# Kernel tuning notes

Measured on AMD Instinct MI355X. Metric: run time of the kernel, lower is better.

Reference implementation:

```python
import jax, jax.numpy as jnp
import numpy as np

HEADS = 8
DIM_HEAD = 32
SCALE = DIM_HEAD ** -0.5


def setup_inputs() -> dict:
    key = jax.random.key(0)
    k1, k2, k3 = jax.random.split(key, 3)
    B, H, W, C = 16, 64, 64, 256
    hidden = HEADS * DIM_HEAD  # 256
    x = jax.random.normal(k1, (B, H, W, C), dtype=jnp.float32)
    # 1x1 convs with no bias == dense matmuls over channel dim (glorot-ish scale)
    w_qkv = jax.random.normal(k2, (C, 3 * hidden), dtype=jnp.float32) * (1.0 / np.sqrt(C))
    w_out = jax.random.normal(k3, (hidden, C), dtype=jnp.float32) * (1.0 / np.sqrt(hidden))
    return {"x": x, "w_qkv": w_qkv, "w_out": w_out}


def reference(x, w_qkv, w_out):
    B, H, W, C = x.shape
    n = H * W
    # to_qkv: 1x1 conv, no bias
    qkv = jnp.einsum('bhwc,cf->bhwf', x, w_qkv)  # [B,H,W,3*hidden]
    q, k, v = jnp.split(qkv, 3, axis=-1)

    def to_heads(t):
        # 'b x y (h c) -> b h c (x y)'
        t = t.reshape(B, n, HEADS, DIM_HEAD)
        return jnp.transpose(t, (0, 2, 3, 1))  # [B, heads, dim_head, n]

    q, k, v = to_heads(q), to_heads(k), to_heads(v)
    q = jax.nn.softmax(q, axis=-2) * SCALE      # softmax over feature dim d
    k = jax.nn.softmax(k, axis=-1)              # softmax over spatial dim n
    context = jnp.einsum('bhdn,bhen->bhde', k, v)   # [B, heads, d, e]
    out = jnp.einsum('bhde,bhdn->bhen', context, q)  # [B, heads, e, n]
    # 'b h c (x y) -> b x y (h c)'
    out = jnp.transpose(out, (0, 3, 1, 2)).reshape(B, H, W, HEADS * DIM_HEAD)
    # to_out: 1x1 conv, no bias
    return jnp.einsum('bhwf,fc->bhwc', out, w_out)
```

## Files before the change

### kernel.cpp

```cpp
#include <hip/hip_runtime.h>

using short8 = __attribute__((ext_vector_type(8))) short;
using f32x4  = __attribute__((ext_vector_type(4))) float;

#define SCALE_Q 0.17677669529663687f
#define NCHUNK 16

__device__ __forceinline__ unsigned short f2bf(float f) {
  unsigned u = __float_as_uint(f);
  return (unsigned short)((u + 0x7FFFu + ((u >> 16) & 1u)) >> 16);
}
__device__ __forceinline__ float bf2f(unsigned h) { return __uint_as_float(h << 16); }

__device__ __forceinline__ void bf8_to_f(uint4 r, float* o) {
  o[0] = bf2f(r.x & 0xffffu); o[1] = bf2f(r.x >> 16);
  o[2] = bf2f(r.y & 0xffffu); o[3] = bf2f(r.y >> 16);
  o[4] = bf2f(r.z & 0xffffu); o[5] = bf2f(r.z >> 16);
  o[6] = bf2f(r.w & 0xffffu); o[7] = bf2f(r.w >> 16);
}

__global__ __launch_bounds__(256) void prep_kernel(
    const float* __restrict__ x, const float* __restrict__ wqkv, const float* __restrict__ wout,
    unsigned short* __restrict__ xb, unsigned short* __restrict__ wqkvT,
    unsigned short* __restrict__ woutT) {
  const int blk = blockIdx.x;
  if (blk < 16384) {
    const size_t i = ((size_t)blk * 256 + threadIdx.x) * 4;
    const float4 v = *(const float4*)(x + i);
    *(ushort4*)(xb + i) = make_ushort4(f2bf(v.x), f2bf(v.y), f2bf(v.z), f2bf(v.w));
  } else if (blk < 16384 + 768) {
    const int n = blk - 16384, k = threadIdx.x;
    wqkvT[n * 256 + k] = f2bf(wqkv[(size_t)k * 768 + n]);
  } else {
    const int c = blk - 16384 - 768, f = threadIdx.x;
    woutT[c * 256 + f] = f2bf(wout[(size_t)f * 256 + c]);
  }
}

__global__ __launch_bounds__(256) void gemm_qkv(
    const unsigned short* __restrict__ A, const unsigned short* __restrict__ BT,
    unsigned short* __restrict__ KV, unsigned short* __restrict__ QS) {
  constexpr int K = 256;
  __shared__ unsigned short As[128][40];
  __shared__ unsigned short Bs[128][40];
  const int cpx = (int)gridDim.x >> 3;
  const int lin = ((int)blockIdx.x & 7) * cpx + ((int)blockIdx.x >> 3);
  const int bn = lin % 6, bm = lin / 6;
  const int tid = threadIdx.x, lane = tid & 63, wid = tid >> 6;
  const int wr = wid >> 1, wc = wid & 1;
  const int fr = lane & 15, hi = lane >> 4, fk = hi * 8;
  f32x4 acc[4][4] = {};
  const size_t abase = (size_t)bm * 128 * K;
  const size_t bbase = (size_t)bn * 128 * K;

#pragma unroll
  for (int kt = 0; kt < K; kt += 32) {
#pragma unroll
    for (int c = tid; c < 512; c += 256) {
      const int row = c >> 2, kc = (c & 3) * 8;
      *(uint4*)&As[row][kc] = *(const uint4*)(A + abase + (size_t)row * K + kt + kc);
      *(uint4*)&Bs[row][kc] = *(const uint4*)(BT + bbase + (size_t)row * K + kt + kc);
    }
    __syncthreads();
    short8 af[4], bfv[4];
#pragma unroll
    for (int i = 0; i < 4; ++i) {
      af[i]  = *(const short8*)&As[wr * 64 + i * 16 + fr][fk];
      bfv[i] = *(const short8*)&Bs[wc * 64 + i * 16 + fr][fk];
    }
#pragma unroll
    for (int mi = 0; mi < 4; ++mi)
#pragma unroll
      for (int nj = 0; nj < 4; ++nj)
        acc[mi][nj] = __builtin_amdgcn_mfma_f32_16x16x32_bf16(bfv[nj], af[mi], acc[mi][nj], 0, 0, 0);
    __syncthreads();
  }

  const size_t r0 = (size_t)bm * 128 + wr * 64;
  if (bn < 2) {
    const int c0 = bn * 128 + wc * 64;
#pragma unroll
    for (int mi = 0; mi < 4; ++mi) {
      const size_t row = r0 + mi * 16 + fr;
#pragma unroll
      for (int p = 0; p < 2; ++p) {
        const f32x4 a0 = acc[mi][2 * p], a1 = acc[mi][2 * p + 1];
        float mx = fmaxf(fmaxf(fmaxf(a0[0], a0[1]), fmaxf(a0[2], a0[3])),
                         fmaxf(fmaxf(a1[0], a1[1]), fmaxf(a1[2], a1[3])));
        mx = fmaxf(mx, __shfl_xor(mx, 16, 64));
        mx = fmaxf(mx, __shfl_xor(mx, 32, 64));
        float e0[4], e1[4], s = 0.f;
#pragma unroll
        for (int r = 0; r < 4; ++r) {
          e0[r] = __expf(a0[r] - mx); e1[r] = __expf(a1[r] - mx);
          s += e0[r] + e1[r];
        }
        s += __shfl_xor(s, 16, 64);
        s += __shfl_xor(s, 32, 64);
        const float inv = SCALE_Q / s;
        unsigned short* qp = QS + row * 256 + c0 + p * 32 + hi * 4;
        *(ushort4*)(qp)      = make_ushort4(f2bf(e0[0]*inv), f2bf(e0[1]*inv), f2bf(e0[2]*inv), f2bf(e0[3]*inv));
        *(ushort4*)(qp + 16) = make_ushort4(f2bf(e1[0]*inv), f2bf(e1[1]*inv), f2bf(e1[2]*inv), f2bf(e1[3]*inv));
      }
    }
    return;
  }
  const int colbase = (bn - 2) * 128 + wc * 64;
#pragma unroll
  for (int mi = 0; mi < 4; ++mi) {
    const size_t row = r0 + mi * 16 + fr;
#pragma unroll
    for (int nj = 0; nj < 4; ++nj) {
      const int col0 = colbase + nj * 16 + hi * 4;
      const f32x4 v = acc[mi][nj];
      *(ushort4*)(KV + row * 512 + col0) =
          make_ushort4(f2bf(v[0]), f2bf(v[1]), f2bf(v[2]), f2bf(v[3]));
    }
  }
}

__global__ __launch_bounds__(256) void gemm_out(
    const unsigned short* __restrict__ A, const unsigned short* __restrict__ BT,
    float* __restrict__ D) {
  constexpr int K = 256;
  __shared__ unsigned short As[128][40];
  __shared__ unsigned short Bs[128][40];
  const int bn = blockIdx.x, bm = blockIdx.y, bz = blockIdx.z;
  const int tid = threadIdx.x, lane = tid & 63, wid = tid >> 6;
  const int wr = wid >> 1, wc = wid & 1;
  const int fr = lane & 15, hi = lane >> 4, fk = hi * 8;
  f32x4 acc[4][4] = {};
  const size_t abase = (size_t)bz * 4096 * 256 + (size_t)bm * 128 * K;
  const size_t bbase = (size_t)bz * 256 * 256 + (size_t)bn * 128 * K;

#pragma unroll
  for (int kt = 0; kt < K; kt += 32) {
#pragma unroll
    for (int c = tid; c < 512; c += 256) {
      const int row = c >> 2, kc = (c & 3) * 8;
      *(uint4*)&As[row][kc] = *(const uint4*)(A + abase + (size_t)row * K + kt + kc);
      *(uint4*)&Bs[row][kc] = *(const uint4*)(BT + bbase + (size_t)row * K + kt + kc);
    }
    __syncthreads();
    short8 af[4], bfv[4];
#pragma unroll
    for (int i = 0; i < 4; ++i) {
      af[i]  = *(const short8*)&As[wr * 64 + i * 16 + fr][fk];
      bfv[i] = *(const short8*)&Bs[wc * 64 + i * 16 + fr][fk];
    }
#pragma unroll
    for (int mi = 0; mi < 4; ++mi)
#pragma unroll
      for (int nj = 0; nj < 4; ++nj)
        acc[mi][nj] = __builtin_amdgcn_mfma_f32_16x16x32_bf16(bfv[nj], af[mi], acc[mi][nj], 0, 0, 0);
    __syncthreads();
  }

  const size_t r0 = (size_t)bm * 128 + wr * 64;
  const int colbase = bn * 128 + wc * 64;
  float* Dz = D + (size_t)bz * 4096 * 256;
#pragma unroll
  for (int mi = 0; mi < 4; ++mi) {
    const size_t row = r0 + mi * 16 + fr;
#pragma unroll
    for (int nj = 0; nj < 4; ++nj) {
      const f32x4 v = acc[mi][nj];
      *(float4*)(Dz + row * 256 + colbase + nj * 16 + hi * 4) =
          make_float4(v[0], v[1], v[2], v[3]);
    }
  }
}

__global__ __launch_bounds__(256) void ctx_part_kernel(const unsigned short* __restrict__ kv,
                                                       float* __restrict__ part,
                                                       float* __restrict__ spart) {
  const int blk = blockIdx.x;
  const int bh = blk >> 4, chunk = blk & 15;
  const int b = bh >> 3, h = bh & 7;
  const int tid = threadIdx.x, d = tid & 31, g = tid >> 5;
  const unsigned short* kbase =
      kv + (size_t)b * 4096 * 512 + h * 32 + (size_t)chunk * 256 * 512;
  const unsigned short* vbase = kbase + 256;

  __shared__ float ek[64][36], vv[64][36];
  float a0 = 0.f, a1 = 0.f, a2 = 0.f, a3 = 0.f, ssum = 0.f;
  const int e0 = g * 4;
  const int sn = tid >> 2, sc = (tid & 3) * 8;
  const unsigned short* kp0 = kbase + (size_t)sn * 512 + sc;
  const unsigned short* vp0 = vbase + (size_t)sn * 512 + sc;
  uint4 kr = *(const uint4*)kp0;
  uint4 vr = *(const uint4*)vp0;
  for (int n0 = 0; n0 < 256; n0 += 64) {
    float kf[8], vf[8];
    bf8_to_f(kr, kf); bf8_to_f(vr, vf);
    uint4 krn = kr, vrn = vr;
    if (n0 + 64 < 256) {
      krn = *(const uint4*)(kp0 + (size_t)(n0 + 64) * 512);
      vrn = *(const uint4*)(vp0 + (size_t)(n0 + 64) * 512);
    }
#pragma unroll
    for (int j = 0; j < 8; ++j) { ek[sn][sc + j] = __expf(kf[j]); vv[sn][sc + j] = vf[j]; }
    __syncthreads();
#pragma unroll 8
    for (int i = 0; i < 64; ++i) {
      const float kd = ek[i][d];
      const float4 v4 = *(const float4*)&vv[i][e0];
      ssum += kd;
      a0 += kd * v4.x; a1 += kd * v4.y; a2 += kd * v4.z; a3 += kd * v4.w;
    }
    __syncthreads();
    kr = krn; vr = vrn;
  }
  float* pp = part + ((size_t)chunk * 128 + bh) * 1024 + d * 32 + e0;
  pp[0] = a0; pp[1] = a1; pp[2] = a2; pp[3] = a3;
  if (g == 0) spart[((size_t)chunk * 128 + bh) * 32 + d] = ssum;
}

__global__ __launch_bounds__(256) void ctx_combine_kernel(const float* __restrict__ part,
                                                          const float* __restrict__ spart,
                                                          float* __restrict__ ctx) {
  const int bh = blockIdx.x, tid = threadIdx.x;
  __shared__ float sinv[32];
  if (tid < 32) {
    float s = 0.f;
#pragma unroll
    for (int c = 0; c < NCHUNK; ++c) s += spart[((size_t)c * 128 + bh) * 32 + tid];
    sinv[tid] = 1.0f / s;
  }
  __syncthreads();
  float4 acc = make_float4(0.f, 0.f, 0.f, 0.f);
#pragma unroll
  for (int c = 0; c < NCHUNK; ++c) {
    const float4 p = *(const float4*)(part + ((size_t)c * 128 + bh) * 1024 + tid * 4);
    acc.x += p.x; acc.y += p.y; acc.z += p.z; acc.w += p.w;
  }
  const float si = sinv[tid >> 3];
  float4* cp = (float4*)(ctx + (size_t)bh * 1024 + tid * 4);
  *cp = make_float4(acc.x * si, acc.y * si, acc.z * si, acc.w * si);
}

__global__ __launch_bounds__(256) void w2_kernel(const float* __restrict__ ctx,
                                                 const unsigned short* __restrict__ woutT,
                                                 unsigned short* __restrict__ W2T) {
  const int b = blockIdx.x >> 4, cg = blockIdx.x & 15;
  const int tid = threadIdx.x;
  __shared__ float cs[8 * 32 * 32];
  {
    const float4* src = (const float4*)(ctx + (size_t)b * 8192);
    float4* dst = (float4*)cs;
#pragma unroll
    for (int i = 0; i < 8; ++i) dst[tid + i * 256] = src[tid + i * 256];
  }
  __syncthreads();
  const int c = cg * 16 + (tid >> 4), chunk = tid & 15;
  const int h = chunk >> 1, d0 = (chunk & 1) * 16;
  float wf[32];
  {
    const uint4* wp = (const uint4*)(woutT + (size_t)c * 256 + h * 32);
    bf8_to_f(wp[0], wf + 0); bf8_to_f(wp[1], wf + 8);
    bf8_to_f(wp[2], wf + 16); bf8_to_f(wp[3], wf + 24);
  }
  unsigned short o[16];
#pragma unroll
  for (int dd = 0; dd < 16; ++dd) {
    const float* cp = cs + h * 1024 + (d0 + dd) * 32;
    float acc = 0.f;
#pragma unroll
    for (int e = 0; e < 32; ++e) acc += cp[e] * wf[e];
    o[dd] = f2bf(acc);
  }
  uint4* op = (uint4*)(W2T + ((size_t)b * 256 + c) * 256 + chunk * 16);
  op[0] = make_uint4((unsigned)o[0] | ((unsigned)o[1] << 16), (unsigned)o[2] | ((unsigned)o[3] << 16),
                     (unsigned)o[4] | ((unsigned)o[5] << 16), (unsigned)o[6] | ((unsigned)o[7] << 16));
  op[1] = make_uint4((unsigned)o[8] | ((unsigned)o[9] << 16), (unsigned)o[10] | ((unsigned)o[11] << 16),
                     (unsigned)o[12] | ((unsigned)o[13] << 16), (unsigned)o[14] | ((unsigned)o[15] << 16));
}

extern "C" void kernel_launch(void* const* d_in, const int* in_sizes, int n_in,
                              void* d_out, int out_size, void* d_ws, size_t ws_size,
                              hipStream_t stream) {
  const float* x     = (const float*)d_in[0];
  const float* wqkv  = (const float*)d_in[1];
  const float* wout  = (const float*)d_in[2];
  float* out = (float*)d_out;

  char* ws = (char*)d_ws;
  unsigned short* xb    = (unsigned short*)(ws);
  unsigned short* wqkvT = (unsigned short*)(ws + 33554432);
  unsigned short* woutT = (unsigned short*)(ws + 33947648);
  unsigned short* kv    = (unsigned short*)(ws + 34078720);
  float*          ctx   = (float*)        (ws + 101187584);
  unsigned short* qs    = (unsigned short*)(ws + 101711872);
  float*          part  = (float*)(ws);
  float*          spart = (float*)(ws + 8388608);
  unsigned short* W2T   = (unsigned short*)(ws + 12582912);

  prep_kernel<<<16384 + 768 + 256, 256, 0, stream>>>(x, wqkv, wout, xb, wqkvT, woutT);
  gemm_qkv<<<3072, 256, 0, stream>>>(xb, wqkvT, kv, qs);
  ctx_part_kernel<<<2048, 256, 0, stream>>>(kv, part, spart);
  ctx_combine_kernel<<<128, 256, 0, stream>>>(part, spart, ctx);
  w2_kernel<<<256, 256, 0, stream>>>(ctx, woutT, W2T);
  gemm_out<<<dim3(2, 32, 16), 256, 0, stream>>>(qs, W2T, out);
}
```

Measured before the change: 178.0 us.

## Double-buffer LDS tiles in both GEMMs with register prefetch of next K-tile

Both bf16 MFMA GEMMs now keep two LDS buffers and load the next K-slice from global memory into registers while the MFMAs run on the current slice. The registers are written to the other buffer afterwards, leaving one barrier per iteration instead of two. K becomes a runtime argument, so the K loop is no longer fully unrolled at compile time, and LDS use per block doubles, which may lower occupancy.

```diff
diff --git a/kernel.cpp b/kernel.cpp
--- a/kernel.cpp
+++ b/kernel.cpp
@@ -39,10 +39,9 @@
 
 __global__ __launch_bounds__(256) void gemm_qkv(
     const unsigned short* __restrict__ A, const unsigned short* __restrict__ BT,
-    unsigned short* __restrict__ KV, unsigned short* __restrict__ QS) {
-  constexpr int K = 256;
-  __shared__ unsigned short As[128][40];
-  __shared__ unsigned short Bs[128][40];
+    unsigned short* __restrict__ KV, unsigned short* __restrict__ QS, int K) {
+  __shared__ unsigned short As[2][128][40];
+  __shared__ unsigned short Bs[2][128][40];
   const int cpx = (int)gridDim.x >> 3;
   const int lin = ((int)blockIdx.x & 7) * cpx + ((int)blockIdx.x >> 3);
   const int bn = lin % 6, bm = lin / 6;
@@ -53,27 +52,42 @@
   const size_t abase = (size_t)bm * 128 * K;
   const size_t bbase = (size_t)bn * 128 * K;
 
-#pragma unroll
-  for (int kt = 0; kt < K; kt += 32) {
-#pragma unroll
-    for (int c = tid; c < 512; c += 256) {
-      const int row = c >> 2, kc = (c & 3) * 8;
-      *(uint4*)&As[row][kc] = *(const uint4*)(A + abase + (size_t)row * K + kt + kc);
-      *(uint4*)&Bs[row][kc] = *(const uint4*)(BT + bbase + (size_t)row * K + kt + kc);
-    }
-    __syncthreads();
+  const int srow = tid >> 2, skc = (tid & 3) * 8;
+  uint4 ra0, ra1, rb0, rb1;
+  const unsigned short* Ap = A + abase + (size_t)srow * K + skc;
+  const unsigned short* Bp = BT + bbase + (size_t)srow * K + skc;
+
+  ra0 = *(const uint4*)(Ap);            ra1 = *(const uint4*)(Ap + (size_t)64 * K);
+  rb0 = *(const uint4*)(Bp);            rb1 = *(const uint4*)(Bp + (size_t)64 * K);
+  *(uint4*)&As[0][srow][skc] = ra0;     *(uint4*)&As[0][srow + 64][skc] = ra1;
+  *(uint4*)&Bs[0][srow][skc] = rb0;     *(uint4*)&Bs[0][srow + 64][skc] = rb1;
+  __syncthreads();
+
+  const int ktiles = K >> 5;
+  int cur = 0;
+  for (int t = 0; t < ktiles; ++t) {
+    if (t + 1 < ktiles) {
+      const int kt = (t + 1) * 32;
+      ra0 = *(const uint4*)(Ap + kt);     ra1 = *(const uint4*)(Ap + (size_t)64 * K + kt);
+      rb0 = *(const uint4*)(Bp + kt);     rb1 = *(const uint4*)(Bp + (size_t)64 * K + kt);
+    }
     short8 af[4], bfv[4];
 #pragma unroll
     for (int i = 0; i < 4; ++i) {
-      af[i]  = *(const short8*)&As[wr * 64 + i * 16 + fr][fk];
-      bfv[i] = *(const short8*)&Bs[wc * 64 + i * 16 + fr][fk];
+      af[i]  = *(const short8*)&As[cur][wr * 64 + i * 16 + fr][fk];
+      bfv[i] = *(const short8*)&Bs[cur][wc * 64 + i * 16 + fr][fk];
     }
 #pragma unroll
     for (int mi = 0; mi < 4; ++mi)
 #pragma unroll
       for (int nj = 0; nj < 4; ++nj)
         acc[mi][nj] = __builtin_amdgcn_mfma_f32_16x16x32_bf16(bfv[nj], af[mi], acc[mi][nj], 0, 0, 0);
+    if (t + 1 < ktiles) {
+      *(uint4*)&As[cur ^ 1][srow][skc] = ra0;  *(uint4*)&As[cur ^ 1][srow + 64][skc] = ra1;
+      *(uint4*)&Bs[cur ^ 1][srow][skc] = rb0;  *(uint4*)&Bs[cur ^ 1][srow + 64][skc] = rb1;
+    }
     __syncthreads();
+    cur ^= 1;
   }
 
   const size_t r0 = (size_t)bm * 128 + wr * 64;
@@ -121,10 +135,9 @@
 
 __global__ __launch_bounds__(256) void gemm_out(
     const unsigned short* __restrict__ A, const unsigned short* __restrict__ BT,
-    float* __restrict__ D) {
-  constexpr int K = 256;
-  __shared__ unsigned short As[128][40];
-  __shared__ unsigned short Bs[128][40];
+    float* __restrict__ D, int K) {
+  __shared__ unsigned short As[2][128][40];
+  __shared__ unsigned short Bs[2][128][40];
   const int bn = blockIdx.x, bm = blockIdx.y, bz = blockIdx.z;
   const int tid = threadIdx.x, lane = tid & 63, wid = tid >> 6;
   const int wr = wid >> 1, wc = wid & 1;
@@ -133,27 +146,42 @@
   const size_t abase = (size_t)bz * 4096 * 256 + (size_t)bm * 128 * K;
   const size_t bbase = (size_t)bz * 256 * 256 + (size_t)bn * 128 * K;
 
-#pragma unroll
-  for (int kt = 0; kt < K; kt += 32) {
-#pragma unroll
-    for (int c = tid; c < 512; c += 256) {
-      const int row = c >> 2, kc = (c & 3) * 8;
-      *(uint4*)&As[row][kc] = *(const uint4*)(A + abase + (size_t)row * K + kt + kc);
-      *(uint4*)&Bs[row][kc] = *(const uint4*)(BT + bbase + (size_t)row * K + kt + kc);
-    }
-    __syncthreads();
+  const int srow = tid >> 2, skc = (tid & 3) * 8;
+  uint4 ra0, ra1, rb0, rb1;
+  const unsigned short* Ap = A + abase + (size_t)srow * K + skc;
+  const unsigned short* Bp = BT + bbase + (size_t)srow * K + skc;
+
+  ra0 = *(const uint4*)(Ap);            ra1 = *(const uint4*)(Ap + (size_t)64 * K);
+  rb0 = *(const uint4*)(Bp);            rb1 = *(const uint4*)(Bp + (size_t)64 * K);
+  *(uint4*)&As[0][srow][skc] = ra0;     *(uint4*)&As[0][srow + 64][skc] = ra1;
+  *(uint4*)&Bs[0][srow][skc] = rb0;     *(uint4*)&Bs[0][srow + 64][skc] = rb1;
+  __syncthreads();
+
+  const int ktiles = K >> 5;
+  int cur = 0;
+  for (int t = 0; t < ktiles; ++t) {
+    if (t + 1 < ktiles) {
+      const int kt = (t + 1) * 32;
+      ra0 = *(const uint4*)(Ap + kt);     ra1 = *(const uint4*)(Ap + (size_t)64 * K + kt);
+      rb0 = *(const uint4*)(Bp + kt);     rb1 = *(const uint4*)(Bp + (size_t)64 * K + kt);
+    }
     short8 af[4], bfv[4];
 #pragma unroll
     for (int i = 0; i < 4; ++i) {
-      af[i]  = *(const short8*)&As[wr * 64 + i * 16 + fr][fk];
-      bfv[i] = *(const short8*)&Bs[wc * 64 + i * 16 + fr][fk];
+      af[i]  = *(const short8*)&As[cur][wr * 64 + i * 16 + fr][fk];
+      bfv[i] = *(const short8*)&Bs[cur][wc * 64 + i * 16 + fr][fk];
     }
 #pragma unroll
     for (int mi = 0; mi < 4; ++mi)
 #pragma unroll
       for (int nj = 0; nj < 4; ++nj)
         acc[mi][nj] = __builtin_amdgcn_mfma_f32_16x16x32_bf16(bfv[nj], af[mi], acc[mi][nj], 0, 0, 0);
+    if (t + 1 < ktiles) {
+      *(uint4*)&As[cur ^ 1][srow][skc] = ra0;  *(uint4*)&As[cur ^ 1][srow + 64][skc] = ra1;
+      *(uint4*)&Bs[cur ^ 1][srow][skc] = rb0;  *(uint4*)&Bs[cur ^ 1][srow + 64][skc] = rb1;
+    }
     __syncthreads();
+    cur ^= 1;
   }
 
   const size_t r0 = (size_t)bm * 128 + wr * 64;
@@ -296,9 +324,9 @@
   unsigned short* W2T   = (unsigned short*)(ws + 12582912);
 
   prep_kernel<<<16384 + 768 + 256, 256, 0, stream>>>(x, wqkv, wout, xb, wqkvT, woutT);
-  gemm_qkv<<<3072, 256, 0, stream>>>(xb, wqkvT, kv, qs);
+  gemm_qkv<<<3072, 256, 0, stream>>>(xb, wqkvT, kv, qs, 256);
   ctx_part_kernel<<<2048, 256, 0, stream>>>(kv, part, spart);
   ctx_combine_kernel<<<128, 256, 0, stream>>>(part, spart, ctx);
   w2_kernel<<<256, 256, 0, stream>>>(ctx, woutT, W2T);
-  gemm_out<<<dim3(2, 32, 16), 256, 0, stream>>>(qs, W2T, out);
-}
+  gemm_out<<<dim3(2, 32, 16), 256, 0, stream>>>(qs, W2T, out, 256);
+}
```

Result: faster. 159.5 us (-10.4%).
